# Performance work log

Measured on AMD Instinct MI355X. Metric: run time of the kernel, lower is better.

The kernel has to match this reference:

```python
import jax, jax.numpy as jnp
import numpy as np

N = 100000      # nodes
E = 1600000     # edges (avg degree 16)
IN = 256        # input feature dim
HID = 64        # per-head hidden dim
H = 4           # attention heads
FC = 256        # collator dim (= H*HID here)
OUT = 4         # classes
ALPHA = 0.2     # LeakyReLU slope


def setup_inputs() -> dict:
    key = jax.random.key(0)
    ks = jax.random.split(key, 24)

    def rn(k, shape, fan_in):
        return jax.random.normal(k, shape, jnp.float32) / np.sqrt(fan_in).astype(np.float32)

    x = jax.random.normal(ks[0], (N, IN), jnp.float32)
    # ensure every node appears at least once as a source so the softmax denom is nonzero
    src = jnp.concatenate([jnp.arange(N, dtype=jnp.int32),
                           jax.random.randint(ks[1], (E - N,), 0, N, dtype=jnp.int32)])
    dst = jax.random.randint(ks[2], (E,), 0, N, dtype=jnp.int32)
    edge_index = jnp.stack([src, dst], axis=0)  # [2, E]

    # layer 1 heads (conv1d k=1 == linear): W [H, HID, IN]; a_1/a_2 conv -> vectors + scalar bias
    W1 = rn(ks[3], (H, HID, IN), IN)
    a11_w = rn(ks[4], (H, HID), HID); a11_b = jnp.zeros((H,), jnp.float32)
    a12_w = rn(ks[5], (H, HID), HID); a12_b = jnp.zeros((H,), jnp.float32)
    b1 = jnp.zeros((H, HID), jnp.float32)
    # layer 2 heads: input is H*HID
    W2 = rn(ks[6], (H, HID, H * HID), H * HID)
    a21_w = rn(ks[7], (H, HID), HID); a21_b = jnp.zeros((H,), jnp.float32)
    a22_w = rn(ks[8], (H, HID), HID); a22_b = jnp.zeros((H,), jnp.float32)
    b2 = jnp.zeros((H, HID), jnp.float32)
    # collator + classifier
    Wc = rn(ks[9], (FC, H * HID), H * HID); bc = jnp.zeros((FC,), jnp.float32)
    Wcls = rn(ks[10], (OUT, FC), FC); bcls = jnp.zeros((OUT,), jnp.float32)

    return dict(x=x, edge_index=edge_index,
                W1=W1, a11_w=a11_w, a11_b=a11_b, a12_w=a12_w, a12_b=a12_b, b1=b1,
                W2=W2, a21_w=a21_w, a21_b=a21_b, a22_w=a22_w, a22_b=a22_b, b2=b2,
                Wc=Wc, bc=bc, Wcls=Wcls, bcls=bcls)


def _gat_head(x, src, dst, W, a1w, a1b, a2w, a2b, b):
    h = x @ W.T                              # [N, HID]
    a1 = h @ a1w + a1b                       # [N] per-node src score
    a2 = h @ a2w + a2b                       # [N] per-node dst score
    s = jnp.exp(jax.nn.leaky_relu(a1[src] + a2[dst], ALPHA))   # [E]
    denom = jax.ops.segment_sum(s, src, num_segments=N)        # [N]
    agg = jax.ops.segment_sum(s[:, None] * h[dst], src, num_segments=N)  # [N, HID]
    return agg / denom[:, None] + b


def reference(x, edge_index, W1, a11_w, a11_b, a12_w, a12_b, b1,
              W2, a21_w, a21_b, a22_w, a22_b, b2, Wc, bc, Wcls, bcls):
    src, dst = edge_index[0], edge_index[1]
    h1 = jnp.concatenate(
        [_gat_head(x, src, dst, W1[i], a11_w[i], a11_b[i], a12_w[i], a12_b[i], b1[i])
         for i in range(H)], axis=1)         # [N, H*HID]
    h1 = jax.nn.relu(h1)
    h2 = jnp.concatenate(
        [_gat_head(h1, src, dst, W2[i], a21_w[i], a21_b[i], a22_w[i], a22_b[i], b2[i])
         for i in range(H)], axis=1)         # [N, H*HID]
    feat = jax.nn.relu(h2 @ Wc.T + bc)       # [N, FC]
    return feat @ Wcls.T + bcls              # [N, OUT]
```

## Files before the change

### kernel.cpp

```cpp
#include <hip/hip_runtime.h>
#include <hip/hip_bf16.h>
#include <hip/hip_fp16.h>
#include <stdint.h>

#define H 4
#define HID 64
#define CDIM 256
#define OUTC 4
#define ALPHA 0.2f
#define NW 16
#define MAXB 512
#define TILE1 4096

typedef __attribute__((ext_vector_type(8))) _Float16 f16x8;
typedef __attribute__((ext_vector_type(4))) float f32x4;

__global__ void detect_k(const uint32_t* __restrict__ xw, int* __restrict__ flag) {
    __shared__ int sd[256];
    int t = threadIdx.x;
    int hits = 0;
    for (int i = 0; i < 16; ++i) {
        uint32_t w = xw[t * 16 + i];
        uint32_t ex = (w >> 7) & 0xffu;
        if (ex >= 100u && ex <= 145u) hits++;
    }
    sd[t] = hits;
    __syncthreads();
    for (int s = 128; s > 0; s >>= 1) {
        if (t < s) sd[t] += sd[t + s];
        __syncthreads();
    }
    if (t == 0) *flag = (sd[0] > 3000) ? 1 : 0;
}

struct WPtrs {
    const void* p[NW];
    int sz[NW];
    int off[NW];
};

__global__ void convert_k(WPtrs ptrs, float* __restrict__ outf, __half* __restrict__ outh,
                          const int* __restrict__ flag) {
    int which = blockIdx.y;
    int n = ptrs.sz[which];
    int i = blockIdx.x * 256 + threadIdx.x;
    if (i >= n) return;
    float v;
    if (*flag) v = __bfloat162float(((const __hip_bfloat16*)ptrs.p[which])[i]);
    else       v = ((const float*)ptrs.p[which])[i];
    outf[ptrs.off[which] + i] = v;
    outh[ptrs.off[which] + i] = __float2half(v);
}

__global__ __launch_bounds__(512) void bhist_k(const int* __restrict__ srcI,
                                               int* __restrict__ bucketCnt,
                                               int Ee, int nbuck)
{
    __shared__ int bc[MAXB];
    int t = threadIdx.x;
    bc[t] = 0;
    __syncthreads();
    int base = blockIdx.x * TILE1;
    #pragma unroll
    for (int q = 0; q < 8; ++q) {
        int i = base + q * 512 + t;
        if (i < Ee) atomicAdd(&bc[srcI[i] >> 8], 1);
    }
    __syncthreads();
    if (t < nbuck && bc[t] > 0) atomicAdd(&bucketCnt[t], bc[t]);
}

__global__ __launch_bounds__(512) void bscan_k(
    const int* __restrict__ bucketCnt, int* __restrict__ bucketCur,
    int* __restrict__ bucketStart, int* __restrict__ rowStart,
    int nbuck, int Nn, int Ee)
{
    __shared__ int sd[MAXB];
    int t = threadIdx.x;
    int v = (t < nbuck) ? bucketCnt[t] : 0;
    sd[t] = v;
    __syncthreads();
    for (int off = 1; off < MAXB; off <<= 1) {
        int add = (t >= off) ? sd[t - off] : 0;
        __syncthreads();
        sd[t] += add;
        __syncthreads();
    }
    if (t < nbuck) {
        int excl = sd[t] - v;
        bucketCur[t] = excl;
        bucketStart[t] = excl;
    }
    if (t == 0) { bucketStart[nbuck] = Ee; rowStart[Nn] = Ee; }
}

__global__ __launch_bounds__(512) void pass1_k(
    const int* __restrict__ srcI, const int* __restrict__ dstI,
    int* __restrict__ bucketCur, uint32_t* __restrict__ pairs,
    int Ee, int nbuck)
{
    __shared__ int cntL[MAXB], scanL[MAXB], exclL[MAXB], curL[MAXB], gbaseL[MAXB];
    __shared__ uint32_t sortedV[TILE1];
    __shared__ uint16_t sortedB[TILE1];
    const int t = threadIdx.x;
    const int base = blockIdx.x * TILE1;
    cntL[t] = 0;
    __syncthreads();
    uint32_t vq[8]; int bq[8];
    #pragma unroll
    for (int q = 0; q < 8; ++q) {
        int i = base + q * 512 + t;
        if (i < Ee) {
            int s = srcI[i], d = dstI[i];
            bq[q] = s >> 8;
            vq[q] = ((uint32_t)d << 8) | (uint32_t)(s & 255);
            atomicAdd(&cntL[bq[q]], 1);
        } else bq[q] = -1;
    }
    __syncthreads();
    scanL[t] = cntL[t];
    __syncthreads();
    for (int off = 1; off < MAXB; off <<= 1) {
        int add = (t >= off) ? scanL[t - off] : 0;
        __syncthreads();
        scanL[t] += add;
        __syncthreads();
    }
    int excl = scanL[t] - cntL[t];
    exclL[t] = excl;
    curL[t] = excl;
    if (t < nbuck && cntL[t] > 0)
        gbaseL[t] = atomicAdd(&bucketCur[t], cntL[t]);
    __syncthreads();
    #pragma unroll
    for (int q = 0; q < 8; ++q) {
        if (bq[q] >= 0) {
            int pos = atomicAdd(&curL[bq[q]], 1);
            sortedV[pos] = vq[q];
            sortedB[pos] = (uint16_t)bq[q];
        }
    }
    __syncthreads();
    int tcount = min(TILE1, Ee - base);
    for (int j = t; j < tcount; j += 512) {
        int b = sortedB[j];
        pairs[gbaseL[b] + (j - exclL[b])] = sortedV[j];
    }
}

__global__ __launch_bounds__(256) void pass2_k(
    const uint32_t* __restrict__ pairs, const int* __restrict__ bucketStart,
    int* __restrict__ rowStart, int* __restrict__ colI, int Nn)
{
    __shared__ int ncnt[256], sd[256], lcur[256];
    int b = blockIdx.x, t = threadIdx.x;
    int n0 = b << 8;
    int s = bucketStart[b], e = bucketStart[b + 1];
    ncnt[t] = 0;
    __syncthreads();
    for (int p = s + t; p < e; p += 256)
        atomicAdd(&ncnt[pairs[p] & 255], 1);
    __syncthreads();
    int v = ncnt[t];
    sd[t] = v;
    __syncthreads();
    for (int off = 1; off < 256; off <<= 1) {
        int add = (t >= off) ? sd[t - off] : 0;
        __syncthreads();
        sd[t] += add;
        __syncthreads();
    }
    int start = s + sd[t] - v;
    lcur[t] = start;
    if (n0 + t < Nn) rowStart[n0 + t] = start;
    __syncthreads();
    for (int p = s + t; p < e; p += 256) {
        uint32_t pv = pairs[p];
        int q = atomicAdd(&lcur[pv & 255], 1);
        colI[q] = (int)(pv >> 8);
    }
}

template <int AMODE, int OMODE>
__global__ __launch_bounds__(256) void gemm_k(
    const void* __restrict__ Ap, const __half* __restrict__ B,
    const float* __restrict__ bias, void* __restrict__ Cp, int M,
    const int* __restrict__ flagp,
    const float* __restrict__ a1w, const float* __restrict__ a1b,
    const float* __restrict__ a2w, const float* __restrict__ a2b,
    float* __restrict__ a1v, __half* __restrict__ a2v)
{
    __shared__ __align__(16) char smem[128 * 136 * 2];
    short* As = (short*)smem;
    short* Bs = (short*)(smem + 10240);
    const int tid  = threadIdx.x;
    const int row0 = blockIdx.x * 128;
    const int col0 = blockIdx.y * 128;
    const int wave = tid >> 6, lane = tid & 63;
    const int m0w = (wave & 1) * 64;
    const int n0w = (wave >> 1) * 64;
    const int lm = lane & 15, lg = lane >> 4;
    const int isbf = (AMODE == 0) ? *flagp : 0;

    f32x4 acc[4][4] = {};

    for (int k0 = 0; k0 < CDIM; k0 += 32) {
        #pragma unroll
        for (int l = 0; l < 2; ++l) {
            int c = tid + l * 256;
            int m = c >> 2, kc = c & 3;
            int gr = row0 + m;
            uint4 q = make_uint4(0u, 0u, 0u, 0u);
            if constexpr (AMODE == 1) {
                const __half* A = (const __half*)Ap;
                if (gr < M) q = *(const uint4*)(A + (size_t)gr * CDIM + k0 + kc * 8);
            } else {
                if (gr < M) {
                    __half hv[8];
                    if (isbf) {
                        const uint4 qb = *(const uint4*)((const __hip_bfloat16*)Ap
                                           + (size_t)gr * CDIM + k0 + kc * 8);
                        const uint32_t* w = (const uint32_t*)&qb;
                        #pragma unroll
                        for (int p = 0; p < 4; ++p) {
                            hv[2*p]   = __float2half(__uint_as_float((w[p] & 0xffffu) << 16));
                            hv[2*p+1] = __float2half(__uint_as_float(w[p] & 0xffff0000u));
                        }
                    } else {
                        const float* A = (const float*)Ap + (size_t)gr * CDIM + k0 + kc * 8;
                        const float4 f0 = *(const float4*)A;
                        const float4 f1 = *(const float4*)(A + 4);
                        hv[0]=__float2half(f0.x); hv[1]=__float2half(f0.y);
                        hv[2]=__float2half(f0.z); hv[3]=__float2half(f0.w);
                        hv[4]=__float2half(f1.x); hv[5]=__float2half(f1.y);
                        hv[6]=__float2half(f1.z); hv[7]=__float2half(f1.w);
                    }
                    q = *(uint4*)hv;
                }
            }
            *(uint4*)(&As[m * 40 + kc * 8]) = q;
        }
        #pragma unroll
        for (int l = 0; l < 2; ++l) {
            int c = tid + l * 256;
            int nn = c >> 2, kc = c & 3;
            uint4 q = *(const uint4*)(B + (size_t)(col0 + nn) * CDIM + k0 + kc * 8);
            *(uint4*)(&Bs[nn * 40 + kc * 8]) = q;
        }
        __syncthreads();
        f16x8 af[4], bfr[4];
        #pragma unroll
        for (int i = 0; i < 4; ++i)
            af[i] = *(f16x8*)(&As[(m0w + i * 16 + lm) * 40 + lg * 8]);
        #pragma unroll
        for (int j = 0; j < 4; ++j)
            bfr[j] = *(f16x8*)(&Bs[(n0w + j * 16 + lm) * 40 + lg * 8]);
        #pragma unroll
        for (int i = 0; i < 4; ++i)
            #pragma unroll
            for (int j = 0; j < 4; ++j)
                acc[i][j] = __builtin_amdgcn_mfma_f32_16x16x32_f16(
                    af[i], bfr[j], acc[i][j], 0, 0, 0);
        __syncthreads();
    }

    if constexpr (OMODE == 1) {
        __half (*Cs)[136] = (__half(*)[136])smem;
        #pragma unroll
        for (int i = 0; i < 4; ++i)
            #pragma unroll
            for (int r = 0; r < 4; ++r) {
                int lr = m0w + i * 16 + lg * 4 + r;
                #pragma unroll
                for (int j = 0; j < 4; ++j)
                    Cs[lr][n0w + j * 16 + lm] = __float2half(acc[i][j][r]);
            }
        __syncthreads();
        __half* C = (__half*)Cp;
        #pragma unroll
        for (int l = 0; l < 8; ++l) {
            int c = tid + l * 256;
            int rr = c >> 4, cc = c & 15;
            int gr = row0 + rr;
            if (gr < M)
                *(uint4*)(C + (size_t)gr * CDIM + col0 + cc * 8) = *(uint4*)(&Cs[rr][cc * 8]);
        }
        {
            int row = tid >> 1, hsel = tid & 1;
            int gr = row0 + row;
            if (gr < M) {
                int ghead = (col0 >> 6) + hsel;
                const float* w1 = a1w + ghead * 64;
                const float* w2 = a2w + ghead * 64;
                const uint* cp = (const uint*)&Cs[row][hsel * 64];
                float s1 = 0.f, s2 = 0.f;
                #pragma unroll
                for (int j = 0; j < 32; ++j) {
                    uint u = cp[j];
                    float2 f = __half22float2(*(__half2*)&u);
                    s1 += f.x * w1[2*j] + f.y * w1[2*j+1];
                    s2 += f.x * w2[2*j] + f.y * w2[2*j+1];
                }
                a1v[(size_t)gr * H + ghead] = s1 + a1b[ghead];
                a2v[(size_t)gr * H + ghead] = __float2half(s2 + a2b[ghead]);
            }
        }
    } else {
        const float* Wc4 = a1w;
        float* pcls = a1v;
        const int slot = blockIdx.y * 2 + (wave >> 1);
        float wv[OUTC][4];
        #pragma unroll
        for (int o = 0; o < OUTC; ++o)
            #pragma unroll
            for (int j = 0; j < 4; ++j)
                wv[o][j] = Wc4[o * CDIM + col0 + n0w + j * 16 + lm];
        #pragma unroll
        for (int i = 0; i < 4; ++i)
            #pragma unroll
            for (int r = 0; r < 4; ++r) {
                int grow = row0 + m0w + i * 16 + lg * 4 + r;
                if (grow < M) {
                    float po[OUTC] = {0.f, 0.f, 0.f, 0.f};
                    #pragma unroll
                    for (int j = 0; j < 4; ++j) {
                        int gcol = col0 + n0w + j * 16 + lm;
                        float t = fmaxf(acc[i][j][r] + bias[gcol], 0.f);
                        #pragma unroll
                        for (int o = 0; o < OUTC; ++o)
                            po[o] = fmaf(t, wv[o][j], po[o]);
                    }
                    #pragma unroll
                    for (int m = 1; m < 16; m <<= 1)
                        #pragma unroll
                        for (int o = 0; o < OUTC; ++o)
                            po[o] += __shfl_xor(po[o], m);
                    if (lm < OUTC) {
                        float v = (lm == 0) ? po[0] : (lm == 1) ? po[1]
                                : (lm == 2) ? po[2] : po[3];
                        pcls[((size_t)grow * 4 + slot) * OUTC + lm] = v;
                    }
                }
            }
        (void)Cp;
    }
}

__global__ __launch_bounds__(256) void agg_k(
    const __half* __restrict__ h,
    const float* __restrict__ a1v, const __half* __restrict__ a2v,
    const int* __restrict__ rowStart, const int* __restrict__ colI,
    const float* __restrict__ bias, __half* __restrict__ outp, int relu, int Nn)
{
    int tid = threadIdx.x;
    int wave = tid >> 6, lane = tid & 63;
    int n = blockIdx.x * 4 + wave;
    if (n >= Nn) return;
    int head = lane >> 4;
    int s = rowStart[n], e = rowStart[n + 1];
    float ac0 = 0.f, ac1 = 0.f, ac2 = 0.f, ac3 = 0.f, den = 0.f;
    const __half* hl = h + lane * 4;
    const float a1n = a1v[(size_t)n * H + head];

    for (int p0 = s; p0 < e; p0 += 8) {
        const int cnt = e - p0;
        int d[8]; float a2q[8]; ushort4 u[8];
        #pragma unroll
        for (int q = 0; q < 8; ++q) {
            int p = p0 + ((q < cnt) ? q : 0);
            d[q] = colI[p];
        }
        #pragma unroll
        for (int q = 0; q < 8; ++q) {
            u[q] = *(const ushort4*)(hl + (size_t)d[q] * CDIM);
            a2q[q] = __half2float(a2v[(size_t)d[q] * H + head]);
        }
        #pragma unroll
        for (int q = 0; q < 8; ++q) {
            float z = a1n + a2q[q];
            z = (z > 0.f) ? z : ALPHA * z;
            float svq = (q < cnt) ? __expf(z) : 0.f;
            den += svq;
            ac0 = fmaf(svq, __half2float(__ushort_as_half(u[q].x)), ac0);
            ac1 = fmaf(svq, __half2float(__ushort_as_half(u[q].y)), ac1);
            ac2 = fmaf(svq, __half2float(__ushort_as_half(u[q].z)), ac2);
            ac3 = fmaf(svq, __half2float(__ushort_as_half(u[q].w)), ac3);
        }
    }

    den = (den > 0.f) ? den : 1.f;
    const float4 b4 = *(const float4*)(bias + lane * 4);
    float r0 = ac0 / den + b4.x;
    float r1 = ac1 / den + b4.y;
    float r2 = ac2 / den + b4.z;
    float r3 = ac3 / den + b4.w;
    if (relu) {
        r0 = fmaxf(r0, 0.f); r1 = fmaxf(r1, 0.f);
        r2 = fmaxf(r2, 0.f); r3 = fmaxf(r3, 0.f);
    }
    ushort4 o;
    o.x = __half_as_ushort(__float2half(r0));
    o.y = __half_as_ushort(__float2half(r1));
    o.z = __half_as_ushort(__float2half(r2));
    o.w = __half_as_ushort(__float2half(r3));
    *(ushort4*)(outp + (size_t)n * CDIM + lane * 4) = o;
}

__global__ void cls2_k(const float* __restrict__ pcls, const float* __restrict__ bcls,
                       void* __restrict__ out, int Nn, const int* __restrict__ flagp)
{
    int n = blockIdx.x * 256 + threadIdx.x;
    if (n >= Nn) return;
    const float4 p0 = *(const float4*)(pcls + (size_t)n * 16);
    const float4 p1 = *(const float4*)(pcls + (size_t)n * 16 + 4);
    const float4 p2 = *(const float4*)(pcls + (size_t)n * 16 + 8);
    const float4 p3 = *(const float4*)(pcls + (size_t)n * 16 + 12);
    float r0 = p0.x + p1.x + p2.x + p3.x + bcls[0];
    float r1 = p0.y + p1.y + p2.y + p3.y + bcls[1];
    float r2 = p0.z + p1.z + p2.z + p3.z + bcls[2];
    float r3 = p0.w + p1.w + p2.w + p3.w + bcls[3];
    if (*flagp) {
        __hip_bfloat16* o = (__hip_bfloat16*)out + (size_t)n * OUTC;
        o[0] = __float2bfloat16(r0); o[1] = __float2bfloat16(r1);
        o[2] = __float2bfloat16(r2); o[3] = __float2bfloat16(r3);
    } else {
        float* o = (float*)out + (size_t)n * OUTC;
        o[0] = r0; o[1] = r1; o[2] = r2; o[3] = r3;
    }
}

extern "C" void kernel_launch(void* const* d_in, const int* in_sizes, int n_in,
                              void* d_out, int out_size, void* d_ws, size_t ws_size,
                              hipStream_t stream)
{
    const void* x  = d_in[0];
    const int*  ei = (const int*)d_in[1];

    const int Nn = in_sizes[0] / CDIM;
    const int Ee = in_sizes[1] / 2;
    const int* srcI = ei;
    const int* dstI = ei + Ee;

    char* wsp = (char*)d_ws;
    size_t off = 0;
    auto alloc = [&](size_t bytes) -> void* {
        void* p = wsp + off;
        off += (bytes + 255) & ~(size_t)255;
        return p;
    };
    __half* hA   = (__half*)alloc((size_t)Nn * CDIM * 2);
    __half* hB   = (__half*)alloc((size_t)Nn * CDIM * 2);
    float*  a1v       = (float*)alloc((size_t)Nn * H * 4);
    __half* a2h       = (__half*)alloc((size_t)Nn * H * 2);
    float*  pcls      = (float*)alloc((size_t)Nn * 4 * OUTC * 4);
    int*    rowStart  = (int*)alloc((size_t)(Nn + 1) * 4);
    int*    colI      = (int*)alloc((size_t)Ee * 4);
    uint32_t* pairs   = (uint32_t*)alloc((size_t)Ee * 4);
    int*    bucketCnt   = (int*)alloc(MAXB * 4);
    int*    bucketCur   = (int*)alloc(MAXB * 4);
    int*    bucketStart = (int*)alloc((MAXB + 1) * 4);
    int*    flag      = (int*)alloc(256);
    float*  wconv     = (float*)alloc((size_t)200000 * 4);
    __half* wh        = (__half*)alloc((size_t)200000 * 2);
    (void)ws_size; (void)n_in; (void)out_size;

    detect_k<<<1, 256, 0, stream>>>((const uint32_t*)x, flag);
    WPtrs wp;
    int woff = 0;
    for (int i = 0; i < NW; ++i) {
        wp.p[i] = d_in[2 + i];
        wp.sz[i] = in_sizes[2 + i];
        wp.off[i] = woff;
        woff += in_sizes[2 + i];
    }
    {
        dim3 cgrid(256, NW);
        convert_k<<<cgrid, 256, 0, stream>>>(wp, wconv, wh, flag);
    }
    const float*  a11wf = wconv + wp.off[1];
    const float*  a11bf = wconv + wp.off[2];
    const float*  a12wf = wconv + wp.off[3];
    const float*  a12bf = wconv + wp.off[4];
    const float*  b1f   = wconv + wp.off[5];
    const float*  a21wf = wconv + wp.off[7];
    const float*  a21bf = wconv + wp.off[8];
    const float*  a22wf = wconv + wp.off[9];
    const float*  a22bf = wconv + wp.off[10];
    const float*  b2f   = wconv + wp.off[11];
    const float*  bcf   = wconv + wp.off[13];
    const float*  Wclsf = wconv + wp.off[14];
    const float*  bclsf = wconv + wp.off[15];
    const __half* W1h   = wh + wp.off[0];
    const __half* W2h   = wh + wp.off[6];
    const __half* Wch   = wh + wp.off[12];

    const int NB = (Nn + 255) / 256;
    const int NBUCK = (Nn + 255) >> 8;
    const int TB = (Ee + TILE1 - 1) / TILE1;

    hipMemsetAsync(bucketCnt, 0, MAXB * 4, stream);
    bhist_k<<<TB, 512, 0, stream>>>(srcI, bucketCnt, Ee, NBUCK);
    bscan_k<<<1, 512, 0, stream>>>(bucketCnt, bucketCur, bucketStart, rowStart,
                                   NBUCK, Nn, Ee);
    pass1_k<<<TB, 512, 0, stream>>>(srcI, dstI, bucketCur, pairs, Ee, NBUCK);
    pass2_k<<<NBUCK, 256, 0, stream>>>(pairs, bucketStart, rowStart, colI, Nn);

    dim3 ggrid((Nn + 127) / 128, CDIM / 128);
    const int AB = (Nn + 3) / 4;

    gemm_k<0, 1><<<ggrid, 256, 0, stream>>>(x, W1h, nullptr, hA, Nn, flag,
                                            a11wf, a11bf, a12wf, a12bf, a1v, a2h);
    agg_k<<<AB, 256, 0, stream>>>(hA, a1v, a2h, rowStart, colI, b1f, hB, 1, Nn);

    gemm_k<1, 1><<<ggrid, 256, 0, stream>>>(hB, W2h, nullptr, hA, Nn, flag,
                                            a21wf, a21bf, a22wf, a22bf, a1v, a2h);
    agg_k<<<AB, 256, 0, stream>>>(hA, a1v, a2h, rowStart, colI, b2f, hB, 0, Nn);

    gemm_k<1, 0><<<ggrid, 256, 0, stream>>>(hB, Wch, bcf, nullptr, Nn, flag,
                                            Wclsf, nullptr, nullptr, nullptr,
                                            pcls, nullptr);
    cls2_k<<<NB, 256, 0, stream>>>(pcls, bclsf, d_out, Nn, flag);
}
```

Measured before the change: 641.6 us.

## Double-buffer GEMM LDS tiles using direct global-to-LDS loads

The MFMA GEMM kernel now stages A and B tiles into two alternating LDS buffers, prefetching the next k-slice while computing the current one. For fp16 A and for B it uses global_load_lds to copy straight from global memory into LDS without passing through registers. Out-of-range rows are clamped to the last valid row instead of being zero-filled. The LDS row stride drops from 40 to 32 halves (no padding), which may add bank conflicts on fragment reads, and double buffering raises LDS use.

```diff
diff --git a/kernel.cpp b/kernel.cpp
--- a/kernel.cpp
+++ b/kernel.cpp
@@ -14,6 +14,9 @@
 
 typedef __attribute__((ext_vector_type(8))) _Float16 f16x8;
 typedef __attribute__((ext_vector_type(4))) float f32x4;
+
+#define GLOBAL_AS(p) ((const __attribute__((address_space(1))) void*)(p))
+#define LDS_AS(p)    ((__attribute__((address_space(3))) void*)(p))
 
 __global__ void detect_k(const uint32_t* __restrict__ xw, int* __restrict__ flag) {
     __shared__ int sd[256];
@@ -191,8 +194,6 @@
     float* __restrict__ a1v, __half* __restrict__ a2v)
 {
     __shared__ __align__(16) char smem[128 * 136 * 2];
-    short* As = (short*)smem;
-    short* Bs = (short*)(smem + 10240);
     const int tid  = threadIdx.x;
     const int row0 = blockIdx.x * 128;
     const int col0 = blockIdx.y * 128;
@@ -202,19 +203,31 @@
     const int lm = lane & 15, lg = lane >> 4;
     const int isbf = (AMODE == 0) ? *flagp : 0;
 
+    const __half* A = (const __half*)Ap;
+    const int lrow = wave * 32 + (lane >> 2);
+    const int kcL  = lane & 3;
+    const size_t arow0 = (size_t)min(row0 + lrow,      M - 1) * CDIM;
+    const size_t arow1 = (size_t)min(row0 + lrow + 16, M - 1) * CDIM;
+    const size_t brow0 = (size_t)(col0 + lrow) * CDIM;
+    const size_t brow1 = (size_t)(col0 + lrow + 16) * CDIM;
+
     f32x4 acc[4][4] = {};
 
-    for (int k0 = 0; k0 < CDIM; k0 += 32) {
-        #pragma unroll
-        for (int l = 0; l < 2; ++l) {
-            int c = tid + l * 256;
-            int m = c >> 2, kc = c & 3;
-            int gr = row0 + m;
-            uint4 q = make_uint4(0u, 0u, 0u, 0u);
-            if constexpr (AMODE == 1) {
-                const __half* A = (const __half*)Ap;
-                if (gr < M) q = *(const uint4*)(A + (size_t)gr * CDIM + k0 + kc * 8);
-            } else {
+    auto stageAB = [&](int buf, int k0) {
+        char* Ab = smem + buf * 16384;
+        char* Bb = Ab + 8192;
+        if constexpr (AMODE == 1) {
+            __builtin_amdgcn_global_load_lds(GLOBAL_AS(A + arow0 + k0 + kcL * 8),
+                LDS_AS(Ab + wave * 2048), 16, 0, 0);
+            __builtin_amdgcn_global_load_lds(GLOBAL_AS(A + arow1 + k0 + kcL * 8),
+                LDS_AS(Ab + wave * 2048 + 1024), 16, 0, 0);
+        } else {
+            #pragma unroll
+            for (int l = 0; l < 2; ++l) {
+                int c = tid + l * 256;
+                int m = c >> 2, kc = c & 3;
+                int gr = row0 + m;
+                uint4 q = make_uint4(0u, 0u, 0u, 0u);
                 if (gr < M) {
                     __half hv[8];
                     if (isbf) {
@@ -227,9 +240,9 @@
                             hv[2*p+1] = __float2half(__uint_as_float(w[p] & 0xffff0000u));
                         }
                     } else {
-                        const float* A = (const float*)Ap + (size_t)gr * CDIM + k0 + kc * 8;
-                        const float4 f0 = *(const float4*)A;
-                        const float4 f1 = *(const float4*)(A + 4);
+                        const float* Af = (const float*)Ap + (size_t)gr * CDIM + k0 + kc * 8;
+                        const float4 f0 = *(const float4*)Af;
+                        const float4 f1 = *(const float4*)(Af + 4);
                         hv[0]=__float2half(f0.x); hv[1]=__float2half(f0.y);
                         hv[2]=__float2half(f0.z); hv[3]=__float2half(f0.w);
                         hv[4]=__float2half(f1.x); hv[5]=__float2half(f1.y);
@@ -237,24 +250,29 @@
                     }
                     q = *(uint4*)hv;
                 }
+                *(uint4*)(Ab + m * 64 + kc * 16) = q;
             }
-            *(uint4*)(&As[m * 40 + kc * 8]) = q;
-        }
-        #pragma unroll
-        for (int l = 0; l < 2; ++l) {
-            int c = tid + l * 256;
-            int nn = c >> 2, kc = c & 3;
-            uint4 q = *(const uint4*)(B + (size_t)(col0 + nn) * CDIM + k0 + kc * 8);
-            *(uint4*)(&Bs[nn * 40 + kc * 8]) = q;
-        }
-        __syncthreads();
+        }
+        __builtin_amdgcn_global_load_lds(GLOBAL_AS(B + brow0 + k0 + kcL * 8),
+            LDS_AS(Bb + wave * 2048), 16, 0, 0);
+        __builtin_amdgcn_global_load_lds(GLOBAL_AS(B + brow1 + k0 + kcL * 8),
+            LDS_AS(Bb + wave * 2048 + 1024), 16, 0, 0);
+    };
+
+    stageAB(0, 0);
+    __syncthreads();
+    int cur = 0;
+    for (int kt = 0; kt < 8; ++kt) {
+        if (kt < 7) stageAB(cur ^ 1, (kt + 1) * 32);
+        const char* Ab = smem + cur * 16384;
+        const char* Bb = Ab + 8192;
         f16x8 af[4], bfr[4];
         #pragma unroll
         for (int i = 0; i < 4; ++i)
-            af[i] = *(f16x8*)(&As[(m0w + i * 16 + lm) * 40 + lg * 8]);
+            af[i] = *(const f16x8*)(Ab + (m0w + i * 16 + lm) * 64 + lg * 16);
         #pragma unroll
         for (int j = 0; j < 4; ++j)
-            bfr[j] = *(f16x8*)(&Bs[(n0w + j * 16 + lm) * 40 + lg * 8]);
+            bfr[j] = *(const f16x8*)(Bb + (n0w + j * 16 + lm) * 64 + lg * 16);
         #pragma unroll
         for (int i = 0; i < 4; ++i)
             #pragma unroll
@@ -262,6 +280,7 @@
                 acc[i][j] = __builtin_amdgcn_mfma_f32_16x16x32_f16(
                     af[i], bfr[j], acc[i][j], 0, 0, 0);
         __syncthreads();
+        cur ^= 1;
     }
 
     if constexpr (OMODE == 1) {
```

Result: faster. 622.1 us (-3.0%).
